# Performance work log

Measured on AMD Instinct MI355X. Metric: run time of the kernel, lower is better.

The kernel has to match this reference:

```python
import jax, jax.numpy as jnp
import numpy as np
from jax import lax


def setup_inputs() -> dict:
    key = jax.random.key(0)
    ks = jax.random.split(key, 9)
    B, L, d_model = 1, 2048, 1024
    d_inner, d_state, d_conv = 2048, 16, 4

    def g(k, shape, scale):
        return jax.random.normal(k, shape, dtype=jnp.float32) * scale

    return dict(
        x=g(ks[0], (B, L, d_model), 1.0),
        in_proj_w=g(ks[1], (2 * d_inner, d_model), 0.02),   # torch Linear layout (out, in)
        conv_w=g(ks[2], (d_inner, 1, d_conv), 0.1),          # depthwise conv kernel
        conv_b=g(ks[3], (d_inner,), 0.02),
        x_proj_w=g(ks[4], (2 * d_state, d_inner), 0.02),
        dt_proj_w=g(ks[5], (d_inner, d_inner), 0.02),
        dt_proj_b=g(ks[6], (d_inner,), 0.02),
        out_proj_w=g(ks[7], (d_model, d_inner), 0.02),
        A_log=jnp.log(jnp.arange(1, d_state + 1, dtype=jnp.float32)),
        D_param=jnp.ones((d_inner,), dtype=jnp.float32),
    )


def reference(x, in_proj_w, conv_w, conv_b, x_proj_w, dt_proj_w, dt_proj_b,
              out_proj_w, A_log, D_param):
    # x: (B, L, d_model)
    B, L, _ = x.shape
    d_inner = D_param.shape[0]
    d_conv = conv_w.shape[-1]

    xz = x @ in_proj_w.T                       # (B, L, 2*d_inner)
    x_p, z = jnp.split(xz, 2, axis=-1)         # each (B, L, d_inner)

    # causal depthwise conv1d: torch pads d_conv-1 both sides then slices [:L],
    # which equals left-pad d_conv-1 with a valid conv.
    xc = jnp.transpose(x_p, (0, 2, 1))         # (B, d_inner, L)
    xc = lax.conv_general_dilated(
        xc, conv_w, window_strides=(1,), padding=[(d_conv - 1, 0)],
        dimension_numbers=('NCH', 'OIH', 'NCH'), feature_group_count=d_inner)
    xc = xc + conv_b[None, :, None]
    xc = jax.nn.silu(jnp.transpose(xc, (0, 2, 1)))  # (B, L, d_inner)

    # ---- ssm(), mode='tustin'. Note: A_discrete in the original is dead code
    # in tustin mode (never used downstream), so it is omitted.
    dt = jax.nn.softplus(xc @ dt_proj_w.T + dt_proj_b)   # (B, L, d_inner)
    BC = xc @ x_proj_w.T                                 # (B, L, 2*d_state)
    B_ssm, C_ssm = jnp.split(BC, 2, axis=-1)             # (B, L, d_state) each

    # Original: B_disc = dt[...,None] * B_ssm[:, :, None, :]  (B,L,D,N)
    #           y = einsum('bld,bldn->bln', xc, B_disc)
    # This contraction factorizes: sum_d xc*dt is independent of n.
    s = jnp.sum(xc * dt, axis=-1, keepdims=True)          # (B, L, 1)
    y = s * B_ssm                                         # (B, L, d_state)
    y = y * C_ssm                                         # einsum('bln,n->bln', ., ones) * C
    # Original does y.sum(-1) + xc * D; keepdims makes the broadcast well-defined.
    y = jnp.sum(y, axis=-1, keepdims=True) + xc * D_param  # (B, L, d_inner)

    y = y * jax.nn.silu(z)
    return y @ out_proj_w.T                                # (B, L, d_model)
```

## Files before the change

### kernel.cpp

```cpp
#include <hip/hip_runtime.h>
#include <hip/hip_bf16.h>

typedef __attribute__((ext_vector_type(8))) short bf16x8;
typedef __attribute__((ext_vector_type(4))) float f32x4;

__device__ __forceinline__ float b2f(unsigned short u) {
  union { float f; unsigned int i; } v; v.i = ((unsigned int)u) << 16; return v.f;
}
__device__ __forceinline__ unsigned short f2b(float f) {
  __hip_bfloat16 h = __float2bfloat16(f);
  union { __hip_bfloat16 h; unsigned short u; } v; v.h = h; return v.u;
}

#define F32_MAGIC 0x3F800000u

#define GLDS16(g, l)                                                        \
  __builtin_amdgcn_global_load_lds(                                         \
      (const __attribute__((address_space(1))) void*)(g),                   \
      (__attribute__((address_space(3))) void*)(l), 16, 0, 0)

#define POST_BARRIER_FENCE()                  \
  do {                                        \
    asm volatile("" ::: "memory");            \
    __builtin_amdgcn_sched_barrier(0);        \
  } while (0)

__global__ __launch_bounds__(256) void cast4_k(const void* __restrict__ s0, unsigned short* __restrict__ d0,
                                               const void* __restrict__ s1, unsigned short* __restrict__ d1,
                                               const void* __restrict__ s2, unsigned short* __restrict__ d2,
                                               const void* __restrict__ s3, unsigned short* __restrict__ d3,
                                               const unsigned int* __restrict__ dpw) {
  const int i = blockIdx.x * 256 + threadIdx.x;
  const void* s; unsigned short* d; int off;
  if      (i <  262144) { s = s0; d = d0; off = i; }
  else if (i <  786432) { s = s1; d = d1; off = i - 262144; }
  else if (i < 1310720) { s = s2; d = d2; off = i - 786432; }
  else if (i < 1572864) { s = s3; d = d3; off = i - 1310720; }
  else return;
  const bool src_f32 = (dpw[0] == F32_MAGIC);
  bf16x8 o;
  if (src_f32) {
    const float* p = (const float*)s + (size_t)off * 8;
#pragma unroll
    for (int j = 0; j < 8; ++j) o[j] = (short)f2b(p[j]);
  } else {
    o = *(const bf16x8*)((const unsigned short*)s + (size_t)off * 8);
  }
  *(bf16x8*)(d + (size_t)off * 8) = o;
}

__global__ __launch_bounds__(256) void cast_small_k(const void* __restrict__ s0, unsigned short* __restrict__ d0,
                                                    const void* __restrict__ s1, unsigned short* __restrict__ d1,
                                                    const void* __restrict__ s2, unsigned short* __restrict__ d2,
                                                    const void* __restrict__ s3, unsigned short* __restrict__ d3,
                                                    const void* __restrict__ s4, unsigned short* __restrict__ d4,
                                                    const unsigned int* __restrict__ dpw) {
  const int i = blockIdx.x * 256 + threadIdx.x;
  const void* s; unsigned short* d; int off;
  if      (i < 8192) { s = s0; d = d0; off = i; }
  else if (i < 9216) { s = s1; d = d1; off = i - 8192; }
  else if (i < 9472) { s = s2; d = d2; off = i - 9216; }
  else if (i < 9728) { s = s3; d = d3; off = i - 9472; }
  else if (i < 9984) { s = s4; d = d4; off = i - 9728; }
  else return;
  const bool src_f32 = (dpw[0] == F32_MAGIC);
  bf16x8 o;
  if (src_f32) {
    const float* p = (const float*)s + (size_t)off * 8;
#pragma unroll
    for (int j = 0; j < 8; ++j) o[j] = (short)f2b(p[j]);
  } else {
    o = *(const bf16x8*)((const unsigned short*)s + (size_t)off * 8);
  }
  *(bf16x8*)(d + (size_t)off * 8) = o;
}

template <int BM, int BN, int BK, int DEPTH, int MODE, int SWZ, int KSPLIT>
__global__ __launch_bounds__(256) void gemm_nt(const unsigned short* __restrict__ A,
                                               const unsigned short* __restrict__ B,
                                               void* __restrict__ C,
                                               int M, int N, int K, int gx,
                                               const unsigned short* __restrict__ bias,
                                               const unsigned int* __restrict__ dpw) {
  constexpr int CPR = BK / 8;
  constexpr int CPRL = (BK == 128) ? 4 : (BK == 64) ? 3 : 2;
  constexpr int LPS_A = BM * BK / 2048;
  constexpr int LPS_B = BN * BK / 2048;
  constexpr int LPS = LPS_A + LPS_B;
  constexpr int ASTEP = BM * BK * 2;
  constexpr int BSTEP = BN * BK * 2;
  constexpr int WM = BM / 2, WN = BN / 2;
  constexpr int MI = WM / 16, NJ = WN / 16;
  constexpr int KK = BK / 32;

  __shared__ char lds[DEPTH * (ASTEP + BSTEP)];
  constexpr int BBASE = DEPTH * ASTEP;

  int bx, by;
  if (SWZ) {
    const int bid = blockIdx.x;
    const int k8 = bid & 7;
    const int s = bid >> 3;
    const int sq = k8 + 8 * (s >> 6);
    const int sqw = gx >> 3;
    bx = (sq % sqw) * 8 + (s & 7);
    by = (sq / sqw) * 8 + ((s >> 3) & 7);
  } else {
    bx = blockIdx.x;
    by = blockIdx.y;
  }
  const int ksOff = (KSPLIT > 1) ? blockIdx.z * (K / KSPLIT) : 0;

  const int tid = threadIdx.x;
  const int lane = tid & 63;
  const int wave = tid >> 6;
  const int m0 = bx * BM;
  const int n0 = by * BN;
  const int wm = (wave >> 1) * WM;
  const int wn = (wave & 1) * WN;
  const int lr = lane & 15;
  const int lu = lane >> 4;

  auto swz = [](int u, int row) {
    int s2 = u ^ (row & (CPR - 1));
    if (CPR == 4) s2 ^= (row >> 2) & 3;
    return s2 & (CPR - 1);
  };

  f32x4 acc[MI][NJ];
#pragma unroll
  for (int i = 0; i < MI; ++i)
#pragma unroll
    for (int j = 0; j < NJ; ++j) acc[i][j] = (f32x4){0.f, 0.f, 0.f, 0.f};

  const unsigned short* aG[LPS_A];
  const unsigned short* bG[LPS_B];
  int aL[LPS_A], bL[LPS_B];
#pragma unroll
  for (int p = 0; p < LPS_A; ++p) {
    const int c = tid + p * 256;
    const int row = c >> CPRL, u = c & (CPR - 1);
    aG[p] = A + (size_t)(m0 + row) * K + ksOff + swz(u, row) * 8;
    aL[p] = c * 16;
  }
#pragma unroll
  for (int q = 0; q < LPS_B; ++q) {
    const int c = tid + q * 256;
    const int row = c >> CPRL, u = c & (CPR - 1);
    bG[q] = B + (size_t)(n0 + row) * K + ksOff + swz(u, row) * 8;
    bL[q] = c * 16;
  }
  int aR[MI][KK], bR[NJ][KK];
#pragma unroll
  for (int i = 0; i < MI; ++i)
#pragma unroll
    for (int kk = 0; kk < KK; ++kk) {
      const int row = wm + i * 16 + lr;
      aR[i][kk] = (row * BK + swz(kk * 4 + lu, row) * 8) * 2;
    }
#pragma unroll
  for (int j = 0; j < NJ; ++j)
#pragma unroll
    for (int kk = 0; kk < KK; ++kk) {
      const int row = wn + j * 16 + lr;
      bR[j][kk] = (row * BK + swz(kk * 4 + lu, row) * 8) * 2;
    }

  const int nk = K / BK / KSPLIT;

  auto stage = [&](int ab, int bb) {
#pragma unroll
    for (int p = 0; p < LPS_A; ++p) {
      GLDS16(aG[p], lds + ab + aL[p]);
      aG[p] += BK;
    }
#pragma unroll
    for (int q = 0; q < LPS_B; ++q) {
      GLDS16(bG[q], lds + BBASE + bb + bL[q]);
      bG[q] += BK;
    }
  };

#pragma unroll
  for (int i = 0; i < DEPTH - 1; ++i)
    if (i < nk) stage(i * ASTEP, i * BSTEP);

  int acb = 0, bcb = 0;
  int asb = (DEPTH - 1) * ASTEP, bsb = (DEPTH - 1) * BSTEP;

  for (int t = 0; t < nk; ++t) {
    const int ahead = nk - 1 - t;
    if (DEPTH >= 4 && ahead >= DEPTH - 2) {
      asm volatile("s_waitcnt vmcnt(%0)" ::"n"((DEPTH - 2) * LPS) : "memory");
    } else if (DEPTH >= 3 && ahead >= 1 && (DEPTH < 4 || ahead == 1)) {
      asm volatile("s_waitcnt vmcnt(%0)" ::"n"(LPS) : "memory");
    } else {
      asm volatile("s_waitcnt vmcnt(0)" ::: "memory");
    }
    __builtin_amdgcn_s_barrier();
    POST_BARRIER_FENCE();

    if (t + DEPTH - 1 < nk) stage(asb, bsb);

#pragma unroll
    for (int kk = 0; kk < KK; ++kk) {
      bf16x8 af[MI], bfr[NJ];
#pragma unroll
      for (int i = 0; i < MI; ++i)
        af[i] = *(const bf16x8*)(lds + acb + aR[i][kk]);
#pragma unroll
      for (int j = 0; j < NJ; ++j)
        bfr[j] = *(const bf16x8*)(lds + BBASE + bcb + bR[j][kk]);
#pragma unroll
      for (int i = 0; i < MI; ++i)
#pragma unroll
        for (int j = 0; j < NJ; ++j)
          acc[i][j] = __builtin_amdgcn_mfma_f32_16x16x32_bf16(af[i], bfr[j], acc[i][j], 0, 0, 0);
    }

    acb = (acb == (DEPTH - 1) * ASTEP) ? 0 : acb + ASTEP;
    bcb = (bcb == (DEPTH - 1) * BSTEP) ? 0 : bcb + BSTEP;
    asb = (asb == (DEPTH - 1) * ASTEP) ? 0 : asb + ASTEP;
    bsb = (bsb == (DEPTH - 1) * BSTEP) ? 0 : bsb + BSTEP;
  }

  const int cr = lu * 4;
  const int cc = lane & 15;
  const bool f32out = (MODE == 2) ? (dpw[0] == F32_MAGIC) : false;
  unsigned short* C16 = (unsigned short*)C +
      ((KSPLIT > 1) ? (size_t)blockIdx.z * (size_t)M * (size_t)N : 0);
#pragma unroll
  for (int i = 0; i < MI; ++i)
#pragma unroll
    for (int j = 0; j < NJ; ++j) {
      const int n = n0 + wn + j * 16 + cc;
#pragma unroll
      for (int r = 0; r < 4; ++r) {
        const size_t off = (size_t)(m0 + wm + i * 16 + cr + r) * N + n;
        float v = acc[i][j][r];
        if (MODE == 0) {
          C16[off] = f2b(v);
        } else {
          if (f32out) ((float*)C)[off] = v;
          else        ((unsigned short*)C)[off] = f2b(v);
        }
      }
    }
}

__global__ __launch_bounds__(256) void gemm_bc_k(const unsigned short* __restrict__ A,
                                                 const unsigned short* __restrict__ B,
                                                 float* __restrict__ C, int K, int Nfull) {
  __shared__ float red[4][16][16];
  const int m0 = blockIdx.x * 16;
  const int n0 = blockIdx.y * 16;
  const int tid = threadIdx.x;
  const int wave = tid >> 6;
  const int lane = tid & 63;
  const int lr = lane & 15;
  const int lk = (lane >> 4) * 8;
  const int kslice = K / 4;

  f32x4 acc = (f32x4){0.f, 0.f, 0.f, 0.f};
  const int kbeg = wave * kslice;
  for (int k0 = kbeg; k0 < kbeg + kslice; k0 += 32) {
    bf16x8 a = *(const bf16x8*)(A + (size_t)(m0 + lr) * K + k0 + lk);
    bf16x8 b = *(const bf16x8*)(B + (size_t)(n0 + lr) * K + k0 + lk);
    acc = __builtin_amdgcn_mfma_f32_16x16x32_bf16(a, b, acc, 0, 0, 0);
  }
  const int cr = (lane >> 4) * 4;
#pragma unroll
  for (int r = 0; r < 4; ++r) red[wave][cr + r][lr] = acc[r];
  __syncthreads();
  if (wave == 0) {
#pragma unroll
    for (int r = 0; r < 4; ++r) {
      float s = red[0][cr + r][lr] + red[1][cr + r][lr] + red[2][cr + r][lr] + red[3][cr + r][lr];
      C[(size_t)(m0 + cr + r) * Nfull + n0 + lr] = s;
    }
  }
}

__global__ __launch_bounds__(256) void conv_silu_k(const unsigned short* __restrict__ xz,
                                                   const unsigned short* __restrict__ cw,
                                                   const unsigned short* __restrict__ cb,
                                                   unsigned short* __restrict__ xc) {
  const int idx = blockIdx.x * 256 + threadIdx.x;
  const int l = idx >> 8;
  const int d0 = (idx & 255) * 8;

  float acc[8];
  bf16x8 bias = *(const bf16x8*)(cb + d0);
#pragma unroll
  for (int j = 0; j < 8; ++j) acc[j] = b2f((unsigned short)bias[j]);

  float wv[32];
#pragma unroll
  for (int q = 0; q < 4; ++q) {
    bf16x8 v = *(const bf16x8*)(cw + (size_t)d0 * 4 + q * 8);
#pragma unroll
    for (int e = 0; e < 8; ++e) wv[q * 8 + e] = b2f((unsigned short)v[e]);
  }

#pragma unroll
  for (int t = 0; t < 4; ++t) {
    const int row = l - 3 + t;
    if (row >= 0) {
      bf16x8 v = *(const bf16x8*)(xz + (size_t)row * 4096 + d0);
#pragma unroll
      for (int j = 0; j < 8; ++j) acc[j] += b2f((unsigned short)v[j]) * wv[j * 4 + t];
    }
  }

  bf16x8 o;
#pragma unroll
  for (int j = 0; j < 8; ++j) {
    float s = acc[j];
    s = s / (1.f + expf(-s));
    o[j] = (short)f2b(s);
  }
  *(bf16x8*)(xc + (size_t)l * 2048 + d0) = o;
}

__global__ __launch_bounds__(256) void combine_k(const unsigned short* __restrict__ dtH,
                                                 const unsigned short* __restrict__ dtb,
                                                 const float* __restrict__ BC,
                                                 unsigned short* __restrict__ xc,
                                                 const unsigned short* __restrict__ xz,
                                                 const unsigned short* __restrict__ Dp) {
  const int l = blockIdx.x;
  const int t = threadIdx.x;
  const int d0 = t * 8;
  const size_t HALF = (size_t)2048 * 2048;

  bf16x8 xcv = *(const bf16x8*)(xc + (size_t)l * 2048 + d0);
  bf16x8 dA = *(const bf16x8*)(dtH + (size_t)l * 2048 + d0);
  bf16x8 dB = *(const bf16x8*)(dtH + HALF + (size_t)l * 2048 + d0);
  bf16x8 dbv = *(const bf16x8*)(dtb + d0);

  float xf[8];
  float s = 0.f;
#pragma unroll
  for (int j = 0; j < 8; ++j) {
    xf[j] = b2f((unsigned short)xcv[j]);
    float pre = b2f((unsigned short)dA[j]) + b2f((unsigned short)dB[j]) + b2f((unsigned short)dbv[j]);
    float dt = (pre > 20.f) ? pre : log1pf(expf(pre));
    s += xf[j] * dt;
  }

#pragma unroll
  for (int off = 32; off > 0; off >>= 1) s += __shfl_down(s, off, 64);

  __shared__ float red[4];
  __shared__ float sb;
  const int lane = t & 63, wv = t >> 6;
  if (lane == 0) red[wv] = s;
  __syncthreads();
  if (t == 0) {
    float ss = red[0] + red[1] + red[2] + red[3];
    float bc = 0.f;
    const float* bcp = BC + (size_t)l * 32;
#pragma unroll
    for (int n = 0; n < 16; ++n) bc += bcp[n] * bcp[16 + n];
    sb = ss * bc;
  }
  __syncthreads();
  const float ypre = sb;

  bf16x8 zv = *(const bf16x8*)(xz + (size_t)l * 4096 + 2048 + d0);
  bf16x8 dv = *(const bf16x8*)(Dp + d0);
  bf16x8 o;
#pragma unroll
  for (int j = 0; j < 8; ++j) {
    float z = b2f((unsigned short)zv[j]);
    float yv = (ypre + xf[j] * b2f((unsigned short)dv[j])) * (z / (1.f + expf(-z)));
    o[j] = (short)f2b(yv);
  }
  *(bf16x8*)(xc + (size_t)l * 2048 + d0) = o;
}

extern "C" void kernel_launch(void* const* d_in, const int* in_sizes, int n_in,
                              void* d_out, int out_size, void* d_ws, size_t ws_size,
                              hipStream_t stream) {
  const void* x_raw   = d_in[0];
  const void* wi_raw  = d_in[1];
  const void* cw_raw  = d_in[2];
  const void* cb_raw  = d_in[3];
  const void* xw_raw  = d_in[4];
  const void* dtw_raw = d_in[5];
  const void* dtb_raw = d_in[6];
  const void* ow_raw  = d_in[7];
  const void* dp_raw  = d_in[9];
  const unsigned int* dpw = (const unsigned int*)dp_raw;

  char* ws = (char*)d_ws;
  const size_t MB = 1u << 20;
  unsigned short* wib  = (unsigned short*)(ws + 0 * MB);
  unsigned short* xb   = (unsigned short*)(ws + 8 * MB);
  unsigned short* dtwb = (unsigned short*)(ws + 16 * MB);
  unsigned short* owb  = (unsigned short*)(ws + 24 * MB);
  unsigned short* xwb  = (unsigned short*)(ws + 28 * MB);
  unsigned short* cwb  = (unsigned short*)(ws + 28 * MB + 256 * 1024);
  unsigned short* cbb  = (unsigned short*)(ws + 28 * MB + 320 * 1024);
  unsigned short* dtbb = (unsigned short*)(ws + 28 * MB + 384 * 1024);
  unsigned short* dpb  = (unsigned short*)(ws + 28 * MB + 448 * 1024);
  unsigned short* xz   = (unsigned short*)(ws + 29 * MB);
  unsigned short* xc   = (unsigned short*)(ws + 45 * MB);
  float*          BC   = (float*)(ws + 53 * MB);
  unsigned short* dtH  = (unsigned short*)(ws + 0 * MB);

  const int L = 2048, DM = 1024, DI = 2048;

  cast4_k<<<6144, 256, 0, stream>>>(x_raw, xb, wi_raw, wib, dtw_raw, dtwb, ow_raw, owb, dpw);
  cast_small_k<<<39, 256, 0, stream>>>(xw_raw, xwb, cw_raw, cwb, cb_raw, cbb,
                                       dtb_raw, dtbb, dp_raw, dpb, dpw);

  gemm_nt<128, 128, 64, 2, 0, 1, 1><<<dim3(16 * 32), 256, 0, stream>>>(xb, wib, xz, L, 2 * DI, DM, 16, nullptr, dpw);
  conv_silu_k<<<dim3(2048), 256, 0, stream>>>(xz, cwb, cbb, xc);
  gemm_nt<128, 128, 64, 2, 0, 0, 2><<<dim3(16, 16, 2), 256, 0, stream>>>(xc, dtwb, dtH, L, DI, DI, 0, nullptr, dpw);
  gemm_bc_k<<<dim3(128, 2), 256, 0, stream>>>(xc, xwb, BC, DI, 32);
  combine_k<<<dim3(2048), 256, 0, stream>>>(dtH, dtbb, BC, xc, xz, dpb);
  gemm_nt<64, 64, 128, 2, 2, 1, 1><<<dim3(32 * 16), 256, 0, stream>>>(xc, owb, d_out, L, DM, DI, 32, nullptr, dpw);
}
```

Baseline: 118.7 us.

## Split-K the output projection into four partials and add a reduction kernel

```diff
diff --git a/kernel.cpp b/kernel.cpp
--- a/kernel.cpp
+++ b/kernel.cpp
@@ -248,6 +248,33 @@
     }
 }
 
+__global__ __launch_bounds__(256) void sum4_k(const unsigned short* __restrict__ p,
+                                              void* __restrict__ out,
+                                              const unsigned int* __restrict__ dpw) {
+  const int i = blockIdx.x * 256 + threadIdx.x;
+  if (i >= 262144) return;
+  const size_t Q = (size_t)2048 * 1024;
+  bf16x8 a = *(const bf16x8*)(p + (size_t)i * 8);
+  bf16x8 b = *(const bf16x8*)(p + Q + (size_t)i * 8);
+  bf16x8 c = *(const bf16x8*)(p + 2 * Q + (size_t)i * 8);
+  bf16x8 d = *(const bf16x8*)(p + 3 * Q + (size_t)i * 8);
+  float r[8];
+#pragma unroll
+  for (int j = 0; j < 8; ++j)
+    r[j] = b2f((unsigned short)a[j]) + b2f((unsigned short)b[j]) +
+           b2f((unsigned short)c[j]) + b2f((unsigned short)d[j]);
+  if (dpw[0] == F32_MAGIC) {
+    float* o = (float*)out + (size_t)i * 8;
+#pragma unroll
+    for (int j = 0; j < 8; ++j) o[j] = r[j];
+  } else {
+    bf16x8 o;
+#pragma unroll
+    for (int j = 0; j < 8; ++j) o[j] = (short)f2b(r[j]);
+    *(bf16x8*)((unsigned short*)out + (size_t)i * 8) = o;
+  }
+}
+
 __global__ __launch_bounds__(256) void gemm_bc_k(const unsigned short* __restrict__ A,
                                                  const unsigned short* __restrict__ B,
                                                  float* __restrict__ C, int K, int Nfull) {
@@ -408,6 +435,7 @@
   unsigned short* xc   = (unsigned short*)(ws + 45 * MB);
   float*          BC   = (float*)(ws + 53 * MB);
   unsigned short* dtH  = (unsigned short*)(ws + 0 * MB);
+  unsigned short* outP = (unsigned short*)(ws + 29 * MB);
 
   const int L = 2048, DM = 1024, DI = 2048;
 
@@ -420,5 +448,6 @@
   gemm_nt<128, 128, 64, 2, 0, 0, 2><<<dim3(16, 16, 2), 256, 0, stream>>>(xc, dtwb, dtH, L, DI, DI, 0, nullptr, dpw);
   gemm_bc_k<<<dim3(128, 2), 256, 0, stream>>>(xc, xwb, BC, DI, 32);
   combine_k<<<dim3(2048), 256, 0, stream>>>(dtH, dtbb, BC, xc, xz, dpb);
-  gemm_nt<64, 64, 128, 2, 2, 1, 1><<<dim3(32 * 16), 256, 0, stream>>>(xc, owb, d_out, L, DM, DI, 32, nullptr, dpw);
-}
+  gemm_nt<128, 128, 64, 2, 0, 0, 4><<<dim3(16, 8, 4), 256, 0, stream>>>(xc, owb, outP, L, DM, DI, 0, nullptr, dpw);
+  sum4_k<<<1024, 256, 0, stream>>>(outP, d_out, dpw);
+}
```

Result: slower. 122.6 us (+3.3%).
